# Kernel optimization log

Hardware: AMD Instinct MI355X
Metric: run time of the kernel (lower is better)

## Reference

```python
import jax, jax.numpy as jnp
import numpy as np

N_NODES = 100000
N_EDGES = 1000000
IN_CH = 312
HID = 256
OUT = 256


def _sage_conv(x, src, dst, W_l, b_l, W_r, num_nodes):
    # PyG SAGEConv (mean aggr): out = mean_{j in N(i)} x_j @ W_l + b_l + x_i @ W_r
    msg = x[src]                                             # [E, C] gather
    agg = jax.ops.segment_sum(msg, dst, num_segments=num_nodes)  # [N, C]
    deg = jax.ops.segment_sum(jnp.ones((src.shape[0],), dtype=x.dtype), dst,
                              num_segments=num_nodes)        # [N]
    mean = agg / jnp.maximum(deg, 1.0)[:, None]
    return mean @ W_l + b_l + x @ W_r


def setup_inputs() -> dict:
    key = jax.random.key(0)
    ks = jax.random.split(key, 8)
    x = jax.random.normal(ks[0], (N_NODES, IN_CH), dtype=jnp.float32)
    edge_index = jax.random.randint(ks[1], (2, N_EDGES), 0, N_NODES, dtype=jnp.int64)
    s1 = 1.0 / np.sqrt(IN_CH)
    s2 = 1.0 / np.sqrt(HID)
    W1_l = jax.random.normal(ks[2], (IN_CH, HID), dtype=jnp.float32) * s1
    b1 = jnp.zeros((HID,), dtype=jnp.float32)
    W1_r = jax.random.normal(ks[3], (IN_CH, HID), dtype=jnp.float32) * s1
    W2_l = jax.random.normal(ks[4], (HID, OUT), dtype=jnp.float32) * s2
    b2 = jnp.zeros((OUT,), dtype=jnp.float32)
    W2_r = jax.random.normal(ks[5], (HID, OUT), dtype=jnp.float32) * s2
    return {"x": x, "edge_index": edge_index, "W1_l": W1_l, "b1": b1,
            "W1_r": W1_r, "W2_l": W2_l, "b2": b2, "W2_r": W2_r}


def reference(x, edge_index, W1_l, b1, W1_r, W2_l, b2, W2_r):
    src, dst = edge_index[0], edge_index[1]
    n = x.shape[0]
    h = _sage_conv(x, src, dst, W1_l, b1, W1_r, n)
    h = jax.nn.relu(h)
    out = _sage_conv(h, src, dst, W2_l, b2, W2_r, n)
    return out
```

## Files before the change

### kernel.cpp

```cpp
#include <hip/hip_runtime.h>
#include <hip/hip_bf16.h>
#include <cstdint>
#include <cstddef>

#define IN_CH 312
#define HID 256

typedef __attribute__((ext_vector_type(8))) short bf16x8;
typedef __attribute__((ext_vector_type(4))) float f32x4;
typedef __attribute__((ext_vector_type(8))) unsigned short ushort8;

__device__ __forceinline__ unsigned short f2bf(float f) {
    union { float f; unsigned u; } v; v.f = f;
    const unsigned r = v.u + 0x7FFFu + ((v.u >> 16) & 1u);
    return (unsigned short)(r >> 16);
}
__device__ __forceinline__ float bf2f(unsigned short s) {
    union { unsigned u; float f; } v; v.u = (unsigned)s << 16;
    return v.f;
}
__device__ __forceinline__ void gload_lds16(const void* g, void* l) {
    __builtin_amdgcn_global_load_lds(
        (const __attribute__((address_space(1))) void*)g,
        (__attribute__((address_space(3))) void*)l, 16, 0, 0);
}

__global__ void detect_idx_kernel(const void* __restrict__ ei, int* __restrict__ flag) {
    if (blockIdx.x == 0 && threadIdx.x == 0) {
        const int* p = (const int*)ei;
        int ok = 1;
        for (int i = 0; i < 64; ++i) ok &= (p[2 * i + 1] == 0);
        *flag = ok;
    }
}
__device__ __forceinline__ long long load_idx(const void* ei, long long i, bool is64) {
    return is64 ? ((const long long*)ei)[i] : (long long)((const int*)ei)[i];
}

__global__ void hist_kernel(const void* __restrict__ ei, const int* __restrict__ flag,
                            int* __restrict__ cnt, int E) {
    const int i = blockIdx.x * blockDim.x + threadIdx.x;
    if (i >= E) return;
    const bool is64 = (*flag != 0);
    atomicAdd(&cnt[load_idx(ei, (long long)E + i, is64)], 1);
}

__global__ void offsets_kernel(const int* __restrict__ cnt, int* __restrict__ counter,
                               int* __restrict__ beg, int* __restrict__ cur, int n) {
    const int i = blockIdx.x * blockDim.x + threadIdx.x;
    if (i >= n) return;
    const int b = atomicAdd(counter, cnt[i]);
    beg[i] = b;
    cur[i] = b;
}

__global__ void fill_kernel(const void* __restrict__ ei, const int* __restrict__ flag,
                            int* __restrict__ cur, int* __restrict__ col, int E) {
    const int i = blockIdx.x * blockDim.x + threadIdx.x;
    if (i >= E) return;
    const bool is64 = (*flag != 0);
    const long long s = load_idx(ei, i, is64);
    const long long d = load_idx(ei, (long long)E + i, is64);
    col[atomicAdd(&cur[d], 1)] = (int)s;
}

__global__ void convert_w_kernel(const float* __restrict__ Wl, const float* __restrict__ Wr,
                                 unsigned short* __restrict__ wt, int K, int Kpad) {
    const int tid = blockIdx.x * blockDim.x + threadIdx.x;
    if (tid >= 512 * Kpad) return;
    const int c = tid / Kpad;
    const int k = tid % Kpad;
    float v = 0.f;
    if (k < K) v = (c < 256) ? Wl[(size_t)k * 256 + c] : Wr[(size_t)k * 256 + (c - 256)];
    wt[(size_t)c * Kpad + k] = f2bf(v);
}

template <int KPAD, bool AFP32, bool ZBF16>
__global__ __launch_bounds__(256) void mfma_gemm_kernel(
    const void* __restrict__ Avoid,
    const unsigned short* __restrict__ WT,
    const float* __restrict__ bias,
    unsigned short* __restrict__ Y,
    void* __restrict__ Z,
    int M)
{
    __shared__ __align__(16) char smem[32768];
    short* a_lds = (short*)smem;
    short* b_lds = (short*)(smem + 16384);

    const int lane = threadIdx.x & 63;
    const int wid  = threadIdx.x >> 6;
    const int wr = wid >> 1, wc = wid & 1;
    const int r0 = blockIdx.x * 128;
    const int c0 = blockIdx.y * 128;

    f32x4 acc[4][4];
    #pragma unroll
    for (int i = 0; i < 4; ++i)
        #pragma unroll
        for (int j = 0; j < 4; ++j) acc[i][j] = (f32x4)0.f;

    const int ldrow  = lane >> 3;
    const int schunk = (lane & 7) ^ ldrow;

    for (int kb = 0; kb < KPAD; kb += 64) {
        __syncthreads();
        #pragma unroll
        for (int j = 0; j < 4; ++j) {
            const int ld = wid * 4 + j;
            const int trow = ld * 8 + ldrow;
            gload_lds16(WT + (size_t)(c0 + trow) * KPAD + kb + schunk * 8,
                        (char*)b_lds + ld * 1024);
        }
        if (AFP32) {
            const float* A = (const float*)Avoid;
            #pragma unroll
            for (int g = 0; g < 2; ++g) {
                float4 v[4];
                #pragma unroll
                for (int it = 0; it < 4; ++it) {
                    const int idx = (int)threadIdx.x + (g * 4 + it) * 256;
                    const int row = idx >> 4, q = idx & 15;
                    const int gr = min(r0 + row, M - 1);
                    const int gk = kb + q * 4;
                    v[it] = (gk < IN_CH) ? *(const float4*)(A + (size_t)gr * IN_CH + gk)
                                         : make_float4(0.f, 0.f, 0.f, 0.f);
                }
                #pragma unroll
                for (int it = 0; it < 4; ++it) {
                    const int idx = (int)threadIdx.x + (g * 4 + it) * 256;
                    const int row = idx >> 4, q = idx & 15;
                    ushort4 b4;
                    b4.x = f2bf(v[it].x); b4.y = f2bf(v[it].y);
                    b4.z = f2bf(v[it].z); b4.w = f2bf(v[it].w);
                    const int byte = row * 128 + (((q >> 1) ^ (row & 7)) * 16) + (q & 1) * 8;
                    *(ushort4*)((char*)a_lds + byte) = b4;
                }
            }
        } else {
            const unsigned short* A = (const unsigned short*)Avoid;
            #pragma unroll
            for (int j = 0; j < 4; ++j) {
                const int ld = wid * 4 + j;
                const int trow = ld * 8 + ldrow;
                const int gr = min(r0 + trow, M - 1);
                gload_lds16(A + (size_t)gr * KPAD + kb + schunk * 8,
                            (char*)a_lds + ld * 1024);
            }
        }
        __syncthreads();

        #pragma unroll
        for (int ks = 0; ks < 2; ++ks) {
            bf16x8 af[4], bg[4];
            #pragma unroll
            for (int f = 0; f < 4; ++f) {
                const int arow = wr * 64 + f * 16 + (lane & 15);
                const int ach  = (ks * 4 + (lane >> 4)) ^ (arow & 7);
                af[f] = *(const bf16x8*)((const char*)a_lds + arow * 128 + ach * 16);
                const int brow = wc * 64 + f * 16 + (lane & 15);
                const int bch  = (ks * 4 + (lane >> 4)) ^ (brow & 7);
                bg[f] = *(const bf16x8*)((const char*)b_lds + brow * 128 + bch * 16);
            }
            #pragma unroll
            for (int fm = 0; fm < 4; ++fm)
                #pragma unroll
                for (int fn = 0; fn < 4; ++fn)
                    acc[fm][fn] = __builtin_amdgcn_mfma_f32_16x16x32_bf16(
                        af[fm], bg[fn], acc[fm][fn], 0, 0, 0);
        }
    }

    const bool isY = (c0 < 256);
    const int cloc = wc * 64 + (lane & 15);

    if (isY || ZBF16) {
        constexpr int CST = 136;
        short* c_lds = (short*)smem;
        float bv4[4];
        #pragma unroll
        for (int fn = 0; fn < 4; ++fn) {
            const int bidx = max(0, c0 - 256) + cloc + fn * 16;
            bv4[fn] = isY ? 0.f : bias[bidx];
        }
        #pragma unroll
        for (int h = 0; h < 2; ++h) {
            __syncthreads();
            if (wr == h) {
                #pragma unroll
                for (int fm = 0; fm < 4; ++fm)
                    #pragma unroll
                    for (int fn = 0; fn < 4; ++fn)
                        #pragma unroll
                        for (int r = 0; r < 4; ++r)
                            c_lds[(fm * 16 + (lane >> 4) * 4 + r) * CST + cloc + fn * 16] =
                                (short)f2bf(acc[fm][fn][r] + bv4[fn]);
            }
            __syncthreads();
            const int row = (int)threadIdx.x >> 2;
            const int cb  = ((int)threadIdx.x & 3) * 32;
            const int gr  = r0 + h * 64 + row;
            if (gr < M) {
                unsigned short* dst = isY
                    ? (Y + (size_t)gr * 256 + c0 + cb)
                    : ((unsigned short*)Z + (size_t)gr * 256 + (c0 - 256) + cb);
                #pragma unroll
                for (int j = 0; j < 4; ++j)
                    *(ushort8*)(dst + j * 8) =
                        *(const ushort8*)&c_lds[row * CST + cb + j * 8];
            }
        }
    } else {
        const int rbase = r0 + wr * 64 + (lane >> 4) * 4;
        #pragma unroll
        for (int fn = 0; fn < 4; ++fn) {
            const int gc = (c0 - 256) + cloc + fn * 16;
            const float bvv = bias[gc];
            #pragma unroll
            for (int fm = 0; fm < 4; ++fm)
                #pragma unroll
                for (int r = 0; r < 4; ++r) {
                    const int gr = rbase + fm * 16 + r;
                    if (gr < M) ((float*)Z)[(size_t)gr * 256 + gc] = acc[fm][fn][r] + bvv;
                }
        }
    }
}

template <bool LAYER1>
__global__ void gather_agg_kernel(const unsigned short* __restrict__ Y,
                                  const int* __restrict__ beg_arr,
                                  const int* __restrict__ cnt,
                                  const int* __restrict__ col,
                                  const void* __restrict__ Z,
                                  void* __restrict__ OUT, int N)
{
    const long long gw = ((long long)blockIdx.x * blockDim.x + threadIdx.x) >> 6;
    if (gw >= N) return;
    const int w = (int)gw;
    const int lane = threadIdx.x & 63;
    const int c4 = lane * 4;
    const int beg = beg_arr[w];
    const int deg = cnt[w];
    const int end = beg + deg;

    float4 a0 = make_float4(0.f, 0.f, 0.f, 0.f);
    float4 a1 = make_float4(0.f, 0.f, 0.f, 0.f);
    int e = beg;
    for (; e + 3 < end; e += 4) {
        const int s0 = col[e], s1 = col[e + 1], s2 = col[e + 2], s3 = col[e + 3];
        const ushort4 v0 = *(const ushort4*)(Y + (size_t)s0 * 256 + c4);
        const ushort4 v1 = *(const ushort4*)(Y + (size_t)s1 * 256 + c4);
        const ushort4 v2 = *(const ushort4*)(Y + (size_t)s2 * 256 + c4);
        const ushort4 v3 = *(const ushort4*)(Y + (size_t)s3 * 256 + c4);
        a0.x += bf2f(v0.x) + bf2f(v1.x);  a1.x += bf2f(v2.x) + bf2f(v3.x);
        a0.y += bf2f(v0.y) + bf2f(v1.y);  a1.y += bf2f(v2.y) + bf2f(v3.y);
        a0.z += bf2f(v0.z) + bf2f(v1.z);  a1.z += bf2f(v2.z) + bf2f(v3.z);
        a0.w += bf2f(v0.w) + bf2f(v1.w);  a1.w += bf2f(v2.w) + bf2f(v3.w);
    }
    for (; e < end; ++e) {
        const ushort4 v0 = *(const ushort4*)(Y + (size_t)col[e] * 256 + c4);
        a0.x += bf2f(v0.x); a0.y += bf2f(v0.y);
        a0.z += bf2f(v0.z); a0.w += bf2f(v0.w);
    }
    float4 acc;
    acc.x = a0.x + a1.x; acc.y = a0.y + a1.y;
    acc.z = a0.z + a1.z; acc.w = a0.w + a1.w;

    const float inv = 1.0f / fmaxf((float)deg, 1.0f);
    float4 z;
    if (LAYER1) {
        const ushort4 zb = *(const ushort4*)((const unsigned short*)Z + (size_t)w * 256 + c4);
        z = make_float4(bf2f(zb.x), bf2f(zb.y), bf2f(zb.z), bf2f(zb.w));
    } else {
        z = *(const float4*)((const float*)Z + (size_t)w * 256 + c4);
    }
    float4 o;
    o.x = acc.x * inv + z.x;
    o.y = acc.y * inv + z.y;
    o.z = acc.z * inv + z.z;
    o.w = acc.w * inv + z.w;
    if (LAYER1) {
        o.x = fmaxf(o.x, 0.f); o.y = fmaxf(o.y, 0.f);
        o.z = fmaxf(o.z, 0.f); o.w = fmaxf(o.w, 0.f);
        ushort4 ob;
        ob.x = f2bf(o.x); ob.y = f2bf(o.y); ob.z = f2bf(o.z); ob.w = f2bf(o.w);
        *(ushort4*)((unsigned short*)OUT + (size_t)w * 256 + c4) = ob;
    } else {
        *(float4*)((float*)OUT + (size_t)w * 256 + c4) = o;
    }
}

extern "C" void kernel_launch(void* const* d_in, const int* in_sizes, int n_in,
                              void* d_out, int out_size, void* d_ws, size_t ws_size,
                              hipStream_t stream) {
    const float* x   = (const float*)d_in[0];
    const void*  ei  = d_in[1];
    const float* W1l = (const float*)d_in[2];
    const float* b1  = (const float*)d_in[3];
    const float* W1r = (const float*)d_in[4];
    const float* W2l = (const float*)d_in[5];
    const float* b2  = (const float*)d_in[6];
    const float* W2r = (const float*)d_in[7];

    const int N = in_sizes[0] / IN_CH;
    const int E = in_sizes[1] / 2;

    char* ws = (char*)d_ws;
    size_t off = 0;
    auto alloc = [&](size_t bytes) {
        void* p = ws + off;
        off = (off + bytes + 255) & ~(size_t)255;
        return p;
    };
    int* flag    = (int*)alloc(4);
    int* cnt     = (int*)alloc((size_t)(N + 1) * 4);
    int* counter = cnt + N;
    int* beg     = (int*)alloc((size_t)N * 4);
    int* cur     = (int*)alloc((size_t)N * 4);
    int* col     = (int*)alloc((size_t)E * 4);
    unsigned short* wt1 = (unsigned short*)alloc((size_t)512 * 320 * 2);
    unsigned short* wt2 = (unsigned short*)alloc((size_t)512 * 256 * 2);
    unsigned short* hb  = (unsigned short*)alloc((size_t)N * 256 * 2);
    unsigned short* y   = (unsigned short*)alloc((size_t)N * 256 * 2);

    float* out = (float*)d_out;
    unsigned short* z1 = (unsigned short*)d_out;

    hipMemsetAsync(cnt, 0, (size_t)(N + 1) * 4, stream);
    detect_idx_kernel<<<1, 64, 0, stream>>>(ei, flag);
    hist_kernel<<<(E + 255) / 256, 256, 0, stream>>>(ei, flag, cnt, E);
    offsets_kernel<<<(N + 255) / 256, 256, 0, stream>>>(cnt, counter, beg, cur, N);
    fill_kernel<<<(E + 255) / 256, 256, 0, stream>>>(ei, flag, cur, col, E);

    convert_w_kernel<<<(512 * 320 + 255) / 256, 256, 0, stream>>>(W1l, W1r, wt1, IN_CH, 320);
    convert_w_kernel<<<(512 * 256 + 255) / 256, 256, 0, stream>>>(W2l, W2r, wt2, HID, 256);

    const dim3 ggrid((N + 127) / 128, 4);

    mfma_gemm_kernel<320, true, true><<<ggrid, 256, 0, stream>>>(x, wt1, b1, y, z1, N);
    gather_agg_kernel<true><<<(N + 3) / 4, 256, 0, stream>>>(y, beg, cnt, col, z1, hb, N);

    mfma_gemm_kernel<256, false, false><<<ggrid, 256, 0, stream>>>(hb, wt2, b2, y, out, N);
    gather_agg_kernel<false><<<(N + 3) / 4, 256, 0, stream>>>(y, beg, cnt, col, out, out, N);
}
```

Baseline: 533.4 us.

## Widen GEMM block tile to 128x256 with 512 threads to halve A-matrix reads

Each GEMM block now computes 128 rows by 256 output columns with 8 waves instead of 128x128 with 4 waves, so the grid's column dimension drops from 4 to 2. Every row tile of the fp32 input x, and of the bf16 hidden activations, is loaded and converted half as many times, which cuts global memory traffic in both layers. In exchange, LDS use grows to 48KB per block and each wave holds a 2x8 accumulator layout. That may lower occupancy, and it halves the number of blocks available to fill the GPU.

Measured after the change: 486.7 us. 8.7% less time.

```diff
diff --git a/kernel.cpp b/kernel.cpp
--- a/kernel.cpp
+++ b/kernel.cpp
@@ -76,7 +76,7 @@
 }
 
 template <int KPAD, bool AFP32, bool ZBF16>
-__global__ __launch_bounds__(256) void mfma_gemm_kernel(
+__global__ __launch_bounds__(512) void mfma_gemm_kernel(
     const void* __restrict__ Avoid,
     const unsigned short* __restrict__ WT,
     const float* __restrict__ bias,
@@ -84,21 +84,22 @@
     void* __restrict__ Z,
     int M)
 {
-    __shared__ __align__(16) char smem[32768];
+    __shared__ __align__(16) char smem[49152];
     short* a_lds = (short*)smem;
     short* b_lds = (short*)(smem + 16384);
 
-    const int lane = threadIdx.x & 63;
-    const int wid  = threadIdx.x >> 6;
+    const int tid  = (int)threadIdx.x;
+    const int lane = tid & 63;
+    const int wid  = tid >> 6;
     const int wr = wid >> 1, wc = wid & 1;
     const int r0 = blockIdx.x * 128;
-    const int c0 = blockIdx.y * 128;
-
-    f32x4 acc[4][4];
+    const int c0 = blockIdx.y * 256;
+
+    f32x4 acc[2][8];
     #pragma unroll
-    for (int i = 0; i < 4; ++i)
-        #pragma unroll
-        for (int j = 0; j < 4; ++j) acc[i][j] = (f32x4)0.f;
+    for (int i = 0; i < 2; ++i)
+        #pragma unroll
+        for (int j = 0; j < 8; ++j) acc[i][j] = (f32x4)0.f;
 
     const int ldrow  = lane >> 3;
     const int schunk = (lane & 7) ^ ldrow;
@@ -114,34 +115,31 @@
         }
         if (AFP32) {
             const float* A = (const float*)Avoid;
-            #pragma unroll
-            for (int g = 0; g < 2; ++g) {
-                float4 v[4];
-                #pragma unroll
-                for (int it = 0; it < 4; ++it) {
-                    const int idx = (int)threadIdx.x + (g * 4 + it) * 256;
-                    const int row = idx >> 4, q = idx & 15;
-                    const int gr = min(r0 + row, M - 1);
-                    const int gk = kb + q * 4;
-                    v[it] = (gk < IN_CH) ? *(const float4*)(A + (size_t)gr * IN_CH + gk)
-                                         : make_float4(0.f, 0.f, 0.f, 0.f);
-                }
-                #pragma unroll
-                for (int it = 0; it < 4; ++it) {
-                    const int idx = (int)threadIdx.x + (g * 4 + it) * 256;
-                    const int row = idx >> 4, q = idx & 15;
-                    ushort4 b4;
-                    b4.x = f2bf(v[it].x); b4.y = f2bf(v[it].y);
-                    b4.z = f2bf(v[it].z); b4.w = f2bf(v[it].w);
-                    const int byte = row * 128 + (((q >> 1) ^ (row & 7)) * 16) + (q & 1) * 8;
-                    *(ushort4*)((char*)a_lds + byte) = b4;
-                }
+            float4 v[4];
+            #pragma unroll
+            for (int it = 0; it < 4; ++it) {
+                const int idx = tid + it * 512;
+                const int row = idx >> 4, q = idx & 15;
+                const int gr = min(r0 + row, M - 1);
+                const int gk = kb + q * 4;
+                v[it] = (gk < IN_CH) ? *(const float4*)(A + (size_t)gr * IN_CH + gk)
+                                     : make_float4(0.f, 0.f, 0.f, 0.f);
+            }
+            #pragma unroll
+            for (int it = 0; it < 4; ++it) {
+                const int idx = tid + it * 512;
+                const int row = idx >> 4, q = idx & 15;
+                ushort4 b4;
+                b4.x = f2bf(v[it].x); b4.y = f2bf(v[it].y);
+                b4.z = f2bf(v[it].z); b4.w = f2bf(v[it].w);
+                const int byte = row * 128 + (((q >> 1) ^ (row & 7)) * 16) + (q & 1) * 8;
+                *(ushort4*)((char*)a_lds + byte) = b4;
             }
         } else {
             const unsigned short* A = (const unsigned short*)Avoid;
             #pragma unroll
-            for (int j = 0; j < 4; ++j) {
-                const int ld = wid * 4 + j;
+            for (int j = 0; j < 2; ++j) {
+                const int ld = wid * 2 + j;
                 const int trow = ld * 8 + ldrow;
                 const int gr = min(r0 + trow, M - 1);
                 gload_lds16(A + (size_t)gr * KPAD + kb + schunk * 8,
@@ -152,58 +150,60 @@
 
         #pragma unroll
         for (int ks = 0; ks < 2; ++ks) {
-            bf16x8 af[4], bg[4];
-            #pragma unroll
-            for (int f = 0; f < 4; ++f) {
-                const int arow = wr * 64 + f * 16 + (lane & 15);
+            bf16x8 af[2], bg[8];
+            #pragma unroll
+            for (int f = 0; f < 2; ++f) {
+                const int arow = wr * 32 + f * 16 + (lane & 15);
                 const int ach  = (ks * 4 + (lane >> 4)) ^ (arow & 7);
                 af[f] = *(const bf16x8*)((const char*)a_lds + arow * 128 + ach * 16);
-                const int brow = wc * 64 + f * 16 + (lane & 15);
+            }
+            #pragma unroll
+            for (int f = 0; f < 8; ++f) {
+                const int brow = wc * 128 + f * 16 + (lane & 15);
                 const int bch  = (ks * 4 + (lane >> 4)) ^ (brow & 7);
                 bg[f] = *(const bf16x8*)((const char*)b_lds + brow * 128 + bch * 16);
             }
             #pragma unroll
-            for (int fm = 0; fm < 4; ++fm)
+            for (int fm = 0; fm < 2; ++fm)
                 #pragma unroll
-                for (int fn = 0; fn < 4; ++fn)
+                for (int fn = 0; fn < 8; ++fn)
                     acc[fm][fn] = __builtin_amdgcn_mfma_f32_16x16x32_bf16(
                         af[fm], bg[fn], acc[fm][fn], 0, 0, 0);
         }
     }
 
-    const bool isY = (c0 < 256);
-    const int cloc = wc * 64 + (lane & 15);
+    const bool isY = (c0 == 0);
+    const int cloc = wc * 128 + (lane & 15);
 
     if (isY || ZBF16) {
-        constexpr int CST = 136;
+        constexpr int CST = 264;
         short* c_lds = (short*)smem;
-        float bv4[4];
-        #pragma unroll
-        for (int fn = 0; fn < 4; ++fn) {
-            const int bidx = max(0, c0 - 256) + cloc + fn * 16;
-            bv4[fn] = isY ? 0.f : bias[bidx];
-        }
+        float bv4[8];
+        #pragma unroll
+        for (int fn = 0; fn < 8; ++fn)
+            bv4[fn] = isY ? 0.f : bias[cloc + fn * 16];
         #pragma unroll
         for (int h = 0; h < 2; ++h) {
             __syncthreads();
-            if (wr == h) {
+            if ((wr >> 1) == h) {
+                const int lr0 = (wr & 1) * 32 + (lane >> 4) * 4;
                 #pragma unroll
-                for (int fm = 0; fm < 4; ++fm)
+                for (int fm = 0; fm < 2; ++fm)
                     #pragma unroll
-                    for (int fn = 0; fn < 4; ++fn)
+                    for (int fn = 0; fn < 8; ++fn)
                         #pragma unroll
                         for (int r = 0; r < 4; ++r)
-                            c_lds[(fm * 16 + (lane >> 4) * 4 + r) * CST + cloc + fn * 16] =
+                            c_lds[(lr0 + fm * 16 + r) * CST + cloc + fn * 16] =
                                 (short)f2bf(acc[fm][fn][r] + bv4[fn]);
             }
             __syncthreads();
-            const int row = (int)threadIdx.x >> 2;
-            const int cb  = ((int)threadIdx.x & 3) * 32;
+            const int row = tid >> 3;
+            const int cb  = (tid & 7) * 32;
             const int gr  = r0 + h * 64 + row;
             if (gr < M) {
                 unsigned short* dst = isY
-                    ? (Y + (size_t)gr * 256 + c0 + cb)
-                    : ((unsigned short*)Z + (size_t)gr * 256 + (c0 - 256) + cb);
+                    ? (Y + (size_t)gr * 256 + cb)
+                    : ((unsigned short*)Z + (size_t)gr * 256 + cb);
                 #pragma unroll
                 for (int j = 0; j < 4; ++j)
                     *(ushort8*)(dst + j * 8) =
@@ -211,13 +211,13 @@
             }
         }
     } else {
-        const int rbase = r0 + wr * 64 + (lane >> 4) * 4;
-        #pragma unroll
-        for (int fn = 0; fn < 4; ++fn) {
-            const int gc = (c0 - 256) + cloc + fn * 16;
+        const int rbase = r0 + wr * 32 + (lane >> 4) * 4;
+        #pragma unroll
+        for (int fn = 0; fn < 8; ++fn) {
+            const int gc = cloc + fn * 16;
             const float bvv = bias[gc];
             #pragma unroll
-            for (int fm = 0; fm < 4; ++fm)
+            for (int fm = 0; fm < 2; ++fm)
                 #pragma unroll
                 for (int r = 0; r < 4; ++r) {
                     const int gr = rbase + fm * 16 + r;
@@ -336,11 +336,11 @@
     convert_w_kernel<<<(512 * 320 + 255) / 256, 256, 0, stream>>>(W1l, W1r, wt1, IN_CH, 320);
     convert_w_kernel<<<(512 * 256 + 255) / 256, 256, 0, stream>>>(W2l, W2r, wt2, HID, 256);
 
-    const dim3 ggrid((N + 127) / 128, 4);
-
-    mfma_gemm_kernel<320, true, true><<<ggrid, 256, 0, stream>>>(x, wt1, b1, y, z1, N);
+    const dim3 ggrid((N + 127) / 128, 2);
+
+    mfma_gemm_kernel<320, true, true><<<ggrid, 512, 0, stream>>>(x, wt1, b1, y, z1, N);
     gather_agg_kernel<true><<<(N + 3) / 4, 256, 0, stream>>>(y, beg, cnt, col, z1, hb, N);
 
-    mfma_gemm_kernel<256, false, false><<<ggrid, 256, 0, stream>>>(hb, wt2, b2, y, out, N);
+    mfma_gemm_kernel<256, false, false><<<ggrid, 512, 0, stream>>>(hb, wt2, b2, y, out, N);
     gather_agg_kernel<false><<<(N + 3) / 4, 256, 0, stream>>>(y, beg, cnt, col, out, out, N);
 }
```
